# Performance work log

Measured on AMD Instinct MI355X. Metric: run time of the kernel, lower is better.

The kernel has to match this reference:

```python
import jax, jax.numpy as jnp
import numpy as np

B, L, G, N, K, E = 64, 512, 128, 32, 8, 65536
NTOK, D_TOK, H_DIR, NTL_INP, NHID, NREL = 10000, 64, 64, 32, 16, 16


def _bn(x, gamma, beta, eps=1e-5):
    # training-mode BatchNorm1d over axis 0; x: (n, C)
    mu = x.mean(0)
    var = x.var(0)
    return gamma * (x - mu) / jnp.sqrt(var + eps) + beta


def _lstm(x, w_ih, w_hh, b_ih, b_hh):
    # x: (B, T, D); torch gate order i, f, g, o
    nb = x.shape[0]
    H = w_hh.shape[1]
    def step(carry, xt):
        h, c = carry
        g = xt @ w_ih.T + b_ih + h @ w_hh.T + b_hh
        i, f, gg, o = jnp.split(g, 4, axis=-1)
        c = jax.nn.sigmoid(f) * c + jax.nn.sigmoid(i) * jnp.tanh(gg)
        h = jax.nn.sigmoid(o) * jnp.tanh(c)
        return (h, c), h
    init = (jnp.zeros((nb, H), x.dtype), jnp.zeros((nb, H), x.dtype))
    _, hs = jax.lax.scan(step, init, jnp.swapaxes(x, 0, 1))
    return jnp.swapaxes(hs, 0, 1)


def setup_inputs() -> dict:
    key = jax.random.key(0)
    ks = jax.random.split(key, 24)
    inp = {}
    inp['seq'] = jax.random.randint(ks[0], (B, L), 0, NTOK)
    inp['pos2grp'] = jax.random.randint(ks[1], (B, L), 0, G)
    inp['idx'] = jax.random.randint(ks[2], (B, N, K), 0, L)
    inp['u'] = jax.random.randint(ks[3], (E,), 0, B * N)
    inp['v'] = jax.random.randint(ks[4], (E,), 0, B * N)
    # parameters
    s = 1.0 / np.sqrt(H_DIR)
    inp['tok_emb'] = jax.random.normal(ks[5], (NTOK, D_TOK), jnp.float32)
    for tag, k0 in (('f', 6), ('b', 10)):
        inp[f'w_ih_{tag}'] = s * jax.random.normal(ks[k0], (4 * H_DIR, D_TOK), jnp.float32)
        inp[f'w_hh_{tag}'] = s * jax.random.normal(ks[k0 + 1], (4 * H_DIR, H_DIR), jnp.float32)
        inp[f'b_ih_{tag}'] = s * jax.random.normal(ks[k0 + 2], (4 * H_DIR,), jnp.float32)
        inp[f'b_hh_{tag}'] = s * jax.random.normal(ks[k0 + 3], (4 * H_DIR,), jnp.float32)
    inp['w_src'] = (1.0 / np.sqrt(2 * H_DIR)) * jax.random.normal(ks[14], (NTL_INP, 2 * H_DIR), jnp.float32)
    inp['b_src'] = jnp.zeros((NTL_INP,), jnp.float32)
    inp['w_dst'] = (1.0 / np.sqrt(2 * H_DIR)) * jax.random.normal(ks[15], (NTL_INP, 2 * H_DIR), jnp.float32)
    inp['b_dst'] = jnp.zeros((NTL_INP,), jnp.float32)
    inp['g_src'] = jnp.ones((NTL_INP,), jnp.float32)
    inp['be_src'] = jnp.zeros((NTL_INP,), jnp.float32)
    inp['g_dst'] = jnp.ones((NTL_INP,), jnp.float32)
    inp['be_dst'] = jnp.zeros((NTL_INP,), jnp.float32)
    inp['ntl_w'] = 0.001 * jax.random.normal(ks[16], (NREL, NHID, NTL_INP, NTL_INP), jnp.float32)
    inp['ntl_v'] = 0.001 * jax.random.normal(ks[17], (NREL, NHID, 2 * NTL_INP), jnp.float32)
    inp['ntl_b'] = jnp.zeros((NREL, NHID, 1), jnp.float32)
    inp['ntl_u'] = 0.001 * jax.random.normal(ks[18], (NREL, 1, NHID), jnp.float32)
    inp['ntl_g'] = jnp.ones((NREL * NHID,), jnp.float32)
    inp['ntl_be'] = jnp.zeros((NREL * NHID,), jnp.float32)
    return inp


def reference(seq, pos2grp, idx, u, v, tok_emb,
              w_ih_f, w_hh_f, b_ih_f, b_hh_f,
              w_ih_b, w_hh_b, b_ih_b, b_hh_b,
              w_src, b_src, w_dst, b_dst,
              g_src, be_src, g_dst, be_dst,
              ntl_w, ntl_v, ntl_b, ntl_u, ntl_g, ntl_be):
    # token embed + scatter-sum tokens -> groups
    x_tok = tok_emb[seq]                                   # (B, L, D)
    gid = (pos2grp + jnp.arange(B)[:, None] * G).reshape(-1)
    x_grp = jax.ops.segment_sum(x_tok.reshape(B * L, -1), gid,
                                num_segments=B * G).reshape(B, G, -1)
    # bidirectional LSTM over groups
    hf = _lstm(x_grp, w_ih_f, w_hh_f, b_ih_f, b_hh_f)
    hb = jnp.flip(_lstm(jnp.flip(x_grp, 1), w_ih_b, w_hh_b, b_ih_b, b_hh_b), 1)
    h_grp = jnp.concatenate([hf, hb], -1)                  # (B, G, 2H)
    # hierarchical gather + sum: node <- sum over K token positions' groups
    b_idx = jnp.arange(B)[:, None, None]
    g_idx = pos2grp[b_idx, idx]                            # (B, N, K)
    h = h_grp[b_idx, g_idx].sum(2).reshape(B * N, -1)      # (B*N, 2H)
    # edge endpoint projections + batchnorm
    hs = _bn(h[u] @ w_src.T + b_src, g_src, be_src)        # (E, ninp)
    ht = _bn(h[v] @ w_dst.T + b_dst, g_dst, be_dst)
    # Neural Tensor Layer
    linear = jnp.einsum('rhd,nd->rhn', ntl_v, jnp.concatenate([hs, ht], 1))
    bil = jnp.stack([
        jnp.einsum('nhj,nj->hn', jnp.einsum('ni,hij->nhj', hs, ntl_w[r]), ht)
        for r in range(NREL)], 0)                          # (R, H, E)
    z = bil + linear + ntl_b
    mu = z.mean(-1, keepdims=True)
    var = z.var(-1, keepdims=True)
    zn = ntl_g.reshape(NREL, NHID, 1) * (z - mu) / jnp.sqrt(var + 1e-5) \
         + ntl_be.reshape(NREL, NHID, 1)
    t = jnp.tanh(zn)
    logit = jnp.einsum('rh,rhn->nr', ntl_u[:, 0, :], t)    # (E, R)
    return logit
```

## Files before the change

kernel.cpp:

```cpp
#include <hip/hip_runtime.h>
#include <hip/hip_bf16.h>
#include <cstdint>

constexpr int B_   = 64;
constexpr int L_   = 512;
constexpr int G_   = 128;
constexpr int N_   = 32;
constexpr int K_   = 8;
constexpr int E_   = 65536;
constexpr int DTOK = 64;
constexpr int H_   = 64;
constexpr int NI   = 32;
constexpr int RH   = 256;
constexpr int M_   = 2048;
constexpr int JA   = 33;
constexpr int COLS = RH * JA;
constexpr int STRD = 36;

#define DEV static __device__ __forceinline__

DEV float sigm(float x) { return 1.f / (1.f + __expf(-x)); }
DEV float tanh_fast(float x) {
    x = fminf(15.f, fmaxf(-15.f, x));
    float e = __expf(2.f * x);
    return (e - 1.f) / (e + 1.f);
}

__global__ __launch_bounds__(256) void k_embed(const int* __restrict__ seq,
                                               const int* __restrict__ p2g,
                                               const float* __restrict__ emb,
                                               float* __restrict__ xg) {
    int gid = blockIdx.x * 256 + threadIdx.x;
    if (gid >= B_ * L_ * DTOK) return;
    int d  = gid & 63;
    int bl = gid >> 6;
    int b  = bl >> 9;
    int s  = seq[bl];
    int g  = p2g[bl];
    atomicAdd(&xg[((b << 7) + g) * 64 + d], emb[s * 64 + d]);
}

__global__ __launch_bounds__(256) void k_hist(const int* __restrict__ u,
                                              const int* __restrict__ v,
                                              int* __restrict__ cu, int* __restrict__ cv) {
    int n = blockIdx.x * 256 + threadIdx.x;
    if (n >= E_) return;
    atomicAdd(&cu[u[n]], 1);
    atomicAdd(&cv[v[n]], 1);
}

__global__ __launch_bounds__(256) void k_pre(const float* __restrict__ xg,
                                             const float* __restrict__ wihf,
                                             const float* __restrict__ bihf,
                                             const float* __restrict__ bhhf,
                                             const float* __restrict__ wihb,
                                             const float* __restrict__ bihb,
                                             const float* __restrict__ bhhb,
                                             float* __restrict__ pre) {
    int dir = blockIdx.y;
    int t   = threadIdx.x;
    const float* wih = dir ? wihb : wihf;
    float bias = dir ? (bihb[t] + bhhb[t]) : (bihf[t] + bhhf[t]);
    int r0 = blockIdx.x * 32;

    float4 wv[16];
#pragma unroll
    for (int c = 0; c < 16; c++) wv[c] = ((const float4*)(wih + t * 64))[c];

    __shared__ __align__(16) float xs[32][68];
    for (int tix = t; tix < 32 * 16; tix += 256) {
        int r = tix >> 4, c = tix & 15;
        ((float4*)&xs[r][0])[c] = ((const float4*)(xg + (size_t)(r0 + r) * 64))[c];
    }
    __syncthreads();

    for (int ml = 0; ml < 32; ml++) {
        float acc = bias;
        const float4* xp = (const float4*)&xs[ml][0];
#pragma unroll
        for (int c = 0; c < 16; c++) {
            float4 x4 = xp[c];
            acc += x4.x * wv[c].x + x4.y * wv[c].y + x4.z * wv[c].z + x4.w * wv[c].w;
        }
        pre[((size_t)dir * 8192 + r0 + ml) * 256 + t] = acc;
    }
}

__global__ __launch_bounds__(256) void k_lstm(const float* __restrict__ pre,
                                              const float* __restrict__ whh_f,
                                              const float* __restrict__ whh_b,
                                              float* __restrict__ hgrp) {
    int blk = blockIdx.x;
    int dir = blk >> 6;
    int b   = blk & 63;
    const float* whh = dir ? whh_b : whh_f;
    int t = threadIdx.x;

    float4 wv[16];
#pragma unroll
    for (int c = 0; c < 16; c++) wv[c] = ((const float4*)(whh + t * 64))[c];

    __shared__ __align__(16) float hl[64];
    __shared__ float cl[64];
    __shared__ float gl[256];
    if (t < 64) { hl[t] = 0.f; cl[t] = 0.f; }
    __syncthreads();

    const float* prow = pre + ((size_t)dir * 8192 + b * G_) * 256 + t;
    int s0 = dir ? (G_ - 1) : 0;
    float pnext = prow[(size_t)s0 * 256];

    for (int k = 0; k < G_; k++) {
        int s = dir ? (G_ - 1 - k) : k;
        float pcur = pnext;
        if (k + 1 < G_) {
            int sn = dir ? (G_ - 2 - k) : (k + 1);
            pnext = prow[(size_t)sn * 256];
        }
        float acc = pcur;
        const float4* hp = (const float4*)hl;
#pragma unroll
        for (int c = 0; c < 16; c++) {
            float4 h4 = hp[c];
            acc += h4.x * wv[c].x + h4.y * wv[c].y + h4.z * wv[c].z + h4.w * wv[c].w;
        }
        gl[t] = acc;
        __syncthreads();
        if (t < 64) {
            float gi = gl[t], gf = gl[64 + t], gg = gl[128 + t], go = gl[192 + t];
            float c2 = sigm(gf) * cl[t] + sigm(gi) * tanh_fast(gg);
            float hh = sigm(go) * tanh_fast(c2);
            cl[t] = c2; hl[t] = hh;
            hgrp[((size_t)b * G_ + s) * 128 + dir * 64 + t] = hh;
        }
        __syncthreads();
    }
}

__global__ __launch_bounds__(128) void k_gather(const int* __restrict__ idx,
                                                const int* __restrict__ p2g,
                                                const float* __restrict__ hgrp,
                                                float* __restrict__ hnode) {
    int m = blockIdx.x;
    int d = threadIdx.x;
    int b = m >> 5;
    float acc = 0.f;
#pragma unroll
    for (int k = 0; k < K_; k++) {
        int l = idx[m * K_ + k];
        int g = p2g[b * L_ + l];
        acc += hgrp[((size_t)b * G_ + g) * 128 + d];
    }
    hnode[(size_t)m * 128 + d] = acc;
}

__global__ __launch_bounds__(256) void k_proj(const float* __restrict__ hnode,
                                              const float* __restrict__ wsrc,
                                              const float* __restrict__ bsrc,
                                              const float* __restrict__ wdst,
                                              const float* __restrict__ bdst,
                                              float* __restrict__ Ps, float* __restrict__ Pd) {
    __shared__ __align__(16) float hsl[8][132];
    __shared__ __align__(16) float wsl[32][132];
    __shared__ __align__(16) float wdl[32][132];
    int m0 = blockIdx.x * 8;
    int t  = threadIdx.x;
    for (int tix = t; tix < 8 * 32; tix += 256) {
        int r = tix >> 5, c = tix & 31;
        ((float4*)&hsl[r][0])[c] = ((const float4*)(hnode + (size_t)(m0 + r) * 128))[c];
    }
    for (int tix = t; tix < 32 * 32; tix += 256) {
        int r = tix >> 5, c = tix & 31;
        ((float4*)&wsl[r][0])[c] = ((const float4*)(wsrc + (size_t)r * 128))[c];
        ((float4*)&wdl[r][0])[c] = ((const float4*)(wdst + (size_t)r * 128))[c];
    }
    __syncthreads();
    int ml = t >> 5, o = t & 31;
    float accS = bsrc[o], accD = bdst[o];
    const float4* hp = (const float4*)&hsl[ml][0];
    const float4* sp = (const float4*)&wsl[o][0];
    const float4* dp = (const float4*)&wdl[o][0];
#pragma unroll
    for (int c = 0; c < 32; c++) {
        float4 h4 = hp[c], s4 = sp[c], d4 = dp[c];
        accS += h4.x * s4.x + h4.y * s4.y + h4.z * s4.z + h4.w * s4.w;
        accD += h4.x * d4.x + h4.y * d4.y + h4.z * d4.z + h4.w * d4.w;
    }
    Ps[(size_t)(m0 + ml) * 32 + o] = accS;
    Pd[(size_t)(m0 + ml) * 32 + o] = accD;
}

__global__ __launch_bounds__(1024) void k_bnstat(const float* __restrict__ Ps,
                                                 const float* __restrict__ Pd,
                                                 const int* __restrict__ cu,
                                                 const int* __restrict__ cv,
                                                 float* __restrict__ bnout) {
    int side = blockIdx.x;
    const float* P  = side ? Pd : Ps;
    const int*   cn = side ? cv : cu;
    int t  = threadIdx.x;
    int mp = t >> 5, o = t & 31;
    float s1 = 0.f, s2 = 0.f;
    for (int m = mp; m < M_; m += 32) {
        float c = (float)cn[m];
        float x = P[(size_t)m * 32 + o];
        s1 += c * x;
        s2 += c * x * x;
    }
    __shared__ float r1[1024], r2[1024];
    r1[t] = s1; r2[t] = s2;
    __syncthreads();
    for (int off = 512; off >= 32; off >>= 1) {
        if (t < off) { r1[t] += r1[t + off]; r2[t] += r2[t + off]; }
        __syncthreads();
    }
    if (t < 32) {
        float mu  = r1[t] / (float)E_;
        float var = r2[t] / (float)E_ - mu * mu;
        bnout[side * 64 + t]      = mu;
        bnout[side * 64 + 32 + t] = rsqrtf(var + 1e-5f);
    }
}

__global__ __launch_bounds__(256) void k_norm(const float* __restrict__ Ps,
                                              const float* __restrict__ Pd,
                                              const float* __restrict__ bnout,
                                              const float* __restrict__ gs,
                                              const float* __restrict__ bes,
                                              const float* __restrict__ gd,
                                              const float* __restrict__ bed,
                                              float* __restrict__ hsaug,
                                              float* __restrict__ htaug) {
    int gid = blockIdx.x * 256 + threadIdx.x;
    if (gid >= M_ * 2 * STRD) return;
    int m = gid / (2 * STRD), s2 = gid % (2 * STRD);
    if (s2 < STRD) {
        int i = s2;
        float val = (i < 32) ? (gs[i] * (Ps[(size_t)m * 32 + i] - bnout[i]) * bnout[32 + i] + bes[i])
                             : ((i == 32) ? 1.f : 0.f);
        hsaug[(size_t)m * STRD + i] = val;
    } else {
        int j = s2 - STRD;
        float val = (j < 32) ? (gd[j] * (Pd[(size_t)m * 32 + j] - bnout[64 + j]) * bnout[96 + j] + bed[j])
                             : ((j == 32) ? 1.f : 0.f);
        htaug[(size_t)m * STRD + j] = val;
    }
}

__global__ __launch_bounds__(256) void k_waug(const float* __restrict__ ntlw,
                                              const float* __restrict__ ntlv,
                                              const float* __restrict__ ntlb,
                                              float* __restrict__ waug) {
    int gid = blockIdx.x * 256 + threadIdx.x;
    if (gid >= JA * COLS) return;
    int i   = gid / COLS;
    int col = gid - i * COLS;
    int rh  = col / JA;
    int j   = col - rh * JA;
    float val;
    if (i < 32) val = (j < 32) ? ntlw[((size_t)rh * 32 + i) * 32 + j] : ntlv[rh * 64 + i];
    else        val = (j == 32) ? ntlb[rh] : 0.f;
    waug[gid] = val;
}

__global__ __launch_bounds__(256) void k_agemm(const float* __restrict__ hsaug,
                                               const float* __restrict__ waug,
                                               __hip_bfloat16* __restrict__ A) {
    int mt  = blockIdx.x;
    int ct  = blockIdx.y;
    int col = ct * 256 + threadIdx.x;
    float w[JA];
#pragma unroll
    for (int i = 0; i < JA; i++) w[i] = waug[(size_t)i * COLS + col];

    __shared__ __align__(16) float hs[32][STRD];
    for (int tix = threadIdx.x; tix < 32 * 9; tix += 256) {
        int r = tix / 9, c = tix - r * 9;
        ((float4*)&hs[r][0])[c] = ((const float4*)(hsaug + (size_t)(mt * 32 + r) * STRD))[c];
    }
    __syncthreads();
#pragma unroll 1
    for (int ml = 0; ml < 32; ml++) {
        float acc = 0.f;
#pragma unroll
        for (int i = 0; i < JA; i++) acc += hs[ml][i] * w[i];
        A[(size_t)(mt * 32 + ml) * COLS + col] = __float2bfloat16(acc);
    }
}

__global__ __launch_bounds__(256) void k_ldst(const float* __restrict__ htaug,
                                              const float* __restrict__ ntlv,
                                              float* __restrict__ Ldst) {
    int m0 = blockIdx.x * 8;
    int rh = threadIdx.x;
    __shared__ __align__(16) float ht[8][STRD];
    for (int tix = threadIdx.x; tix < 8 * 9; tix += 256) {
        int r = tix / 9, c = tix - r * 9;
        ((float4*)&ht[r][0])[c] = ((const float4*)(htaug + (size_t)(m0 + r) * STRD))[c];
    }
    float w[32];
#pragma unroll
    for (int j = 0; j < 32; j++) w[j] = ntlv[rh * 64 + 32 + j];
    __syncthreads();
    for (int ml = 0; ml < 8; ml++) {
        float acc = 0.f;
#pragma unroll
        for (int j = 0; j < 32; j++) acc += ht[ml][j] * w[j];
        Ldst[(size_t)(m0 + ml) * 256 + rh] = acc;
    }
}

__global__ __launch_bounds__(1024) void k_scan(const int* __restrict__ cu,
                                               int* __restrict__ ustart,
                                               int* __restrict__ ucursor) {
    __shared__ int s[2048];
    int t  = threadIdx.x;
    int c0 = cu[t], c1 = cu[t + 1024];
    s[t] = c0; s[t + 1024] = c1;
    __syncthreads();
    for (int off = 1; off < 2048; off <<= 1) {
        int a0 = (t >= off) ? s[t - off] : 0;
        int a1 = ((t + 1024) >= off) ? s[t + 1024 - off] : 0;
        __syncthreads();
        s[t] += a0; s[t + 1024] += a1;
        __syncthreads();
    }
    int e0 = s[t] - c0, e1 = s[t + 1024] - c1;
    ustart[t] = e0;            ustart[t + 1024] = e1;
    ucursor[t] = e0;           ucursor[t + 1024] = e1;
    if (t == 0) ustart[2048] = E_;
}

__global__ __launch_bounds__(256) void k_scatter(const int* __restrict__ u,
                                                 int* __restrict__ ucursor,
                                                 int* __restrict__ eorder) {
    int n = blockIdx.x * 256 + threadIdx.x;
    if (n >= E_) return;
    int pos = atomicAdd(&ucursor[u[n]], 1);
    eorder[pos] = n;
}

__global__ __launch_bounds__(256, 2) void k_z(const __hip_bfloat16* __restrict__ A,
                                              const float* __restrict__ htaug,
                                              const float* __restrict__ Ldst,
                                              const int* __restrict__ ustart,
                                              const int* __restrict__ eorder,
                                              const int* __restrict__ v,
                                              __hip_bfloat16* __restrict__ z,
                                              float* __restrict__ zsum,
                                              float* __restrict__ zsq) {
    __shared__ __align__(16) float al[256 * STRD];
    __shared__ __align__(16) float htl[32][STRD];
    __shared__ int nnl[32], vvl[32];
    int t = threadIdx.x;
    al[t * STRD + 33] = 0.f; al[t * STRD + 34] = 0.f; al[t * STRD + 35] = 0.f;
    float s1 = 0.f, s2 = 0.f;

    for (int ui = 0; ui < 4; ui++) {
        int uu = blockIdx.x * 4 + ui;
        __syncthreads();
        for (int k = 0; k < JA; k++) {
            int idx2 = k * 256 + t;
            int rh = idx2 / JA, j = idx2 - rh * JA;
            al[rh * STRD + j] = __bfloat162float(A[(size_t)uu * COLS + idx2]);
        }
        __syncthreads();
        float4 av4[9];
#pragma unroll
        for (int c = 0; c < 9; c++) av4[c] = ((const float4*)&al[t * STRD])[c];

        int e0 = ustart[uu], e1 = ustart[uu + 1];
        for (int eb = e0; eb < e1; eb += 32) {
            int nb = min(32, e1 - eb);
            __syncthreads();
            if (t < nb) { int n = eorder[eb + t]; nnl[t] = n; vvl[t] = v[n]; }
            __syncthreads();
            for (int tix = t; tix < nb * 9; tix += 256) {
                int e = tix / 9, c = tix - e * 9;
                ((float4*)&htl[e][0])[c] = ((const float4*)(htaug + (size_t)vvl[e] * STRD))[c];
            }
            __syncthreads();
            for (int e = 0; e < nb; e++) {
                float acc = Ldst[(size_t)vvl[e] * 256 + t];
                const float4* hp = (const float4*)&htl[e][0];
#pragma unroll
                for (int c = 0; c < 9; c++) {
                    float4 h4 = hp[c];
                    acc += av4[c].x * h4.x + av4[c].y * h4.y + av4[c].z * h4.z + av4[c].w * h4.w;
                }
                z[(size_t)nnl[e] * 256 + t] = __float2bfloat16(acc);
                s1 += acc; s2 += acc * acc;
            }
        }
    }
    atomicAdd(&zsum[t], s1);
    atomicAdd(&zsq[t], s2);
}

__global__ __launch_bounds__(256) void k_lnfin(const float* __restrict__ zsum,
                                               const float* __restrict__ zsq,
                                               float* __restrict__ zstat) {
    int t = threadIdx.x;
    float mu  = zsum[t] / (float)E_;
    float var = zsq[t] / (float)E_ - mu * mu;
    zstat[t]       = mu;
    zstat[256 + t] = rsqrtf(var + 1e-5f);
}

__global__ __launch_bounds__(256) void k_logit(const __hip_bfloat16* __restrict__ z,
                                               const float* __restrict__ zstat,
                                               const float* __restrict__ ntlu,
                                               const float* __restrict__ ntlg,
                                               const float* __restrict__ ntlbe,
                                               float* __restrict__ out) {
    int t  = threadIdx.x;
    int n0 = blockIdx.x * 16;
    float mu  = zstat[t], isd = zstat[256 + t];
    float g   = ntlg[t],  be  = ntlbe[t];
    float uw  = ntlu[t];
    float zv[16];
#pragma unroll
    for (int nl = 0; nl < 16; nl++)
        zv[nl] = __bfloat162float(z[(size_t)(n0 + nl) * 256 + t]);
#pragma unroll 1
    for (int nl = 0; nl < 16; nl++) {
        float zn  = g * (zv[nl] - mu) * isd + be;
        float val = uw * tanhf(zn);
        val += __shfl_xor(val, 1);
        val += __shfl_xor(val, 2);
        val += __shfl_xor(val, 4);
        val += __shfl_xor(val, 8);
        if ((t & 15) == 0) out[(size_t)(n0 + nl) * 16 + (t >> 4)] = val;
    }
}

extern "C" void kernel_launch(void* const* d_in, const int* in_sizes, int n_in,
                              void* d_out, int out_size, void* d_ws, size_t ws_size,
                              hipStream_t stream) {
    const int*   seq   = (const int*)d_in[0];
    const int*   p2g   = (const int*)d_in[1];
    const int*   idx   = (const int*)d_in[2];
    const int*   u     = (const int*)d_in[3];
    const int*   v     = (const int*)d_in[4];
    const float* emb   = (const float*)d_in[5];
    const float* wihf  = (const float*)d_in[6];
    const float* whhf  = (const float*)d_in[7];
    const float* bihf  = (const float*)d_in[8];
    const float* bhhf  = (const float*)d_in[9];
    const float* wihb  = (const float*)d_in[10];
    const float* whhb  = (const float*)d_in[11];
    const float* bihb  = (const float*)d_in[12];
    const float* bhhb  = (const float*)d_in[13];
    const float* wsrc  = (const float*)d_in[14];
    const float* bsrc  = (const float*)d_in[15];
    const float* wdst  = (const float*)d_in[16];
    const float* bdst  = (const float*)d_in[17];
    const float* gs    = (const float*)d_in[18];
    const float* bes   = (const float*)d_in[19];
    const float* gd    = (const float*)d_in[20];
    const float* bed   = (const float*)d_in[21];
    const float* ntlw  = (const float*)d_in[22];
    const float* ntlv  = (const float*)d_in[23];
    const float* ntlb  = (const float*)d_in[24];
    const float* ntlu  = (const float*)d_in[25];
    const float* ntlg  = (const float*)d_in[26];
    const float* ntlbe = (const float*)d_in[27];
    float* out = (float*)d_out;

    char* ws = (char*)d_ws;
    size_t off = 0;
    auto take = [&](size_t bytes) -> char* {
        char* p = ws + off;
        off = (off + bytes + 255) & ~(size_t)255;
        return p;
    };
    float* x_grp  = (float*)take((size_t)B_ * G_ * 64 * 4);
    int*   cnt_u  = (int*)  take(2048 * 4);
    int*   cnt_v  = (int*)  take(2048 * 4);
    float* zsum   = (float*)take(256 * 4);
    float* zsq    = (float*)take(256 * 4);
    size_t zero_bytes = off;
    int*   ucursor = (int*)  take(2048 * 4);
    int*   ustart  = (int*)  take(2049 * 4);
    int*   eorder  = (int*)  take((size_t)E_ * 4);
    float* pre     = (float*)take((size_t)2 * 8192 * 256 * 4);
    float* hgrp    = (float*)take((size_t)B_ * G_ * 128 * 4);
    float* hnode   = (float*)take((size_t)M_ * 128 * 4);
    float* Psrc    = (float*)take((size_t)M_ * 32 * 4);
    float* Pdst    = (float*)take((size_t)M_ * 32 * 4);
    float* bnout   = (float*)take(128 * 4);
    float* hsaug   = (float*)take((size_t)M_ * STRD * 4);
    float* htaug   = (float*)take((size_t)M_ * STRD * 4);
    float* waug    = (float*)take((size_t)JA * COLS * 4);
    float* LdstB   = (float*)take((size_t)M_ * 256 * 4);
    float* zstat   = (float*)take(512 * 4);
    __hip_bfloat16* Abuf = (__hip_bfloat16*)take((size_t)M_ * COLS * 2);
    __hip_bfloat16* zbuf = (__hip_bfloat16*)take((size_t)E_ * 256 * 2);
    (void)ws_size; (void)in_sizes; (void)n_in; (void)out_size;

    hipMemsetAsync(d_ws, 0, zero_bytes, stream);

    k_embed<<<(B_ * L_ * DTOK) / 256, 256, 0, stream>>>(seq, p2g, emb, x_grp);
    k_hist<<<E_ / 256, 256, 0, stream>>>(u, v, cnt_u, cnt_v);
    k_pre<<<dim3(256, 2), 256, 0, stream>>>(x_grp, wihf, bihf, bhhf, wihb, bihb, bhhb, pre);
    k_lstm<<<128, 256, 0, stream>>>(pre, whhf, whhb, hgrp);
    k_gather<<<M_, 128, 0, stream>>>(idx, p2g, hgrp, hnode);
    k_proj<<<M_ / 8, 256, 0, stream>>>(hnode, wsrc, bsrc, wdst, bdst, Psrc, Pdst);
    k_bnstat<<<2, 1024, 0, stream>>>(Psrc, Pdst, cnt_u, cnt_v, bnout);
    k_norm<<<(M_ * 2 * STRD + 255) / 256, 256, 0, stream>>>(Psrc, Pdst, bnout, gs, bes, gd, bed, hsaug, htaug);
    k_waug<<<(JA * COLS + 255) / 256, 256, 0, stream>>>(ntlw, ntlv, ntlb, waug);
    k_agemm<<<dim3(M_ / 32, JA), 256, 0, stream>>>(hsaug, waug, Abuf);
    k_ldst<<<M_ / 8, 256, 0, stream>>>(htaug, ntlv, LdstB);
    k_scan<<<1, 1024, 0, stream>>>(cnt_u, ustart, ucursor);
    k_scatter<<<E_ / 256, 256, 0, stream>>>(u, ucursor, eorder);
    k_z<<<M_ / 4, 256, 0, stream>>>(Abuf, htaug, LdstB, ustart, eorder, v, zbuf, zsum, zsq);
    k_lnfin<<<1, 256, 0, stream>>>(zsum, zsq, zstat);
    k_logit<<<E_ / 16, 256, 0, stream>>>(zbuf, zstat, ntlu, ntlg, ntlbe, out);
}
```

Baseline: 422.1 us.

## Fuse small kernels, restructure LSTM step with lane permutes, fold ldst into waug

Merges embed+hist, pre+scan, lstm+scatter, norm+waug and lnfin+logit into combined launches, cutting the number of kernel launches. The embedding sum now accumulates per batch in shared memory rather than through global atomics. The LSTM step gathers the four gates through ds_bpermute, keeps the cell state in registers and double-buffers h, so each step needs one barrier instead of two. The destination-linear term is folded into the augmented weight row (the constant-1 column), which removes the Ldst kernel and its buffer. The logit kernel uses the fast tanh approximation, which adds a small accuracy risk.

```diff
diff --git a/kernel.cpp b/kernel.cpp
--- a/kernel.cpp
+++ b/kernel.cpp
@@ -10,7 +10,6 @@
 constexpr int E_   = 65536;
 constexpr int DTOK = 64;
 constexpr int H_   = 64;
-constexpr int NI   = 32;
 constexpr int RH   = 256;
 constexpr int M_   = 2048;
 constexpr int JA   = 33;
@@ -25,28 +24,37 @@
     float e = __expf(2.f * x);
     return (e - 1.f) / (e + 1.f);
 }
-
-__global__ __launch_bounds__(256) void k_embed(const int* __restrict__ seq,
-                                               const int* __restrict__ p2g,
-                                               const float* __restrict__ emb,
-                                               float* __restrict__ xg) {
-    int gid = blockIdx.x * 256 + threadIdx.x;
-    if (gid >= B_ * L_ * DTOK) return;
-    int d  = gid & 63;
-    int bl = gid >> 6;
-    int b  = bl >> 9;
-    int s  = seq[bl];
-    int g  = p2g[bl];
-    atomicAdd(&xg[((b << 7) + g) * 64 + d], emb[s * 64 + d]);
-}
-
-__global__ __launch_bounds__(256) void k_hist(const int* __restrict__ u,
-                                              const int* __restrict__ v,
-                                              int* __restrict__ cu, int* __restrict__ cv) {
-    int n = blockIdx.x * 256 + threadIdx.x;
-    if (n >= E_) return;
-    atomicAdd(&cu[u[n]], 1);
-    atomicAdd(&cv[v[n]], 1);
+DEV float bperm(float x, int srclane) {
+    return __int_as_float(__builtin_amdgcn_ds_bpermute(srclane << 2, __float_as_int(x)));
+}
+
+__global__ __launch_bounds__(256) void k_eh(const int* __restrict__ seq,
+                                            const int* __restrict__ p2g,
+                                            const float* __restrict__ emb,
+                                            const int* __restrict__ u,
+                                            const int* __restrict__ v,
+                                            float* __restrict__ xg,
+                                            int* __restrict__ cu, int* __restrict__ cv) {
+    int blk = blockIdx.x;
+    int t   = threadIdx.x;
+    if (blk >= 64) {
+        int n = (blk - 64) * 256 + t;
+        atomicAdd(&cu[u[n]], 1);
+        atomicAdd(&cv[v[n]], 1);
+        return;
+    }
+    __shared__ float xgl[G_ * 64];
+    for (int i = t; i < G_ * 64; i += 256) xgl[i] = 0.f;
+    __syncthreads();
+    int b = blk;
+    int d = t & 63, part = t >> 6;
+    for (int l = part; l < L_; l += 4) {
+        int s = seq[b * L_ + l];
+        int g = p2g[b * L_ + l];
+        atomicAdd(&xgl[g * 64 + d], emb[s * 64 + d]);
+    }
+    __syncthreads();
+    for (int i = t; i < G_ * 64; i += 256) xg[(size_t)b * G_ * 64 + i] = xgl[i];
 }
 
 __global__ __launch_bounds__(256) void k_pre(const float* __restrict__ xg,
@@ -56,18 +64,44 @@
                                              const float* __restrict__ wihb,
                                              const float* __restrict__ bihb,
                                              const float* __restrict__ bhhb,
-                                             float* __restrict__ pre) {
-    int dir = blockIdx.y;
+                                             float* __restrict__ pre,
+                                             const int* __restrict__ cu,
+                                             int* __restrict__ ustart,
+                                             int* __restrict__ ucursor) {
+    int blk = blockIdx.x;
     int t   = threadIdx.x;
+    __shared__ __align__(16) float xs[32][68];
+    __shared__ int ps[256];
+    if (blk == 512) {
+        int base = t * 8, run = 0;
+        int c[8], loc[8];
+#pragma unroll
+        for (int i = 0; i < 8; i++) c[i] = cu[base + i];
+#pragma unroll
+        for (int i = 0; i < 8; i++) { loc[i] = run; run += c[i]; }
+        ps[t] = run;
+        __syncthreads();
+        for (int off = 1; off < 256; off <<= 1) {
+            int a = (t >= off) ? ps[t - off] : 0;
+            __syncthreads();
+            ps[t] += a;
+            __syncthreads();
+        }
+        int ex = ps[t] - run;
+#pragma unroll
+        for (int i = 0; i < 8; i++) { ustart[base + i] = ex + loc[i]; ucursor[base + i] = ex + loc[i]; }
+        if (t == 255) ustart[2048] = E_;
+        return;
+    }
+    int dir = blk >> 8;
     const float* wih = dir ? wihb : wihf;
     float bias = dir ? (bihb[t] + bhhb[t]) : (bihf[t] + bhhf[t]);
-    int r0 = blockIdx.x * 32;
+    int r0 = (blk & 255) * 32;
 
     float4 wv[16];
 #pragma unroll
     for (int c = 0; c < 16; c++) wv[c] = ((const float4*)(wih + t * 64))[c];
 
-    __shared__ __align__(16) float xs[32][68];
     for (int tix = t; tix < 32 * 16; tix += 256) {
         int r = tix >> 4, c = tix & 15;
         ((float4*)&xs[r][0])[c] = ((const float4*)(xg + (size_t)(r0 + r) * 64))[c];
@@ -86,29 +120,43 @@
     }
 }
 
-__global__ __launch_bounds__(256) void k_lstm(const float* __restrict__ pre,
-                                              const float* __restrict__ whh_f,
-                                              const float* __restrict__ whh_b,
-                                              float* __restrict__ hgrp) {
+__global__ __launch_bounds__(256) void k_ls(const float* __restrict__ pre,
+                                            const float* __restrict__ whh_f,
+                                            const float* __restrict__ whh_b,
+                                            float* __restrict__ hgrp,
+                                            const int* __restrict__ u,
+                                            int* __restrict__ ucursor,
+                                            int* __restrict__ eorder) {
     int blk = blockIdx.x;
+    int t   = threadIdx.x;
+    if (blk >= 128) {
+        int n = (blk - 128) * 256 + t;
+        int pos = atomicAdd(&ucursor[u[n]], 1);
+        eorder[pos] = n;
+        return;
+    }
     int dir = blk >> 6;
     int b   = blk & 63;
     const float* whh = dir ? whh_b : whh_f;
-    int t = threadIdx.x;
+    int l = t & 63;
+    int w = t >> 6;
+    int q = l >> 4;
+    int e = (w << 4) + (l & 15);
+    int grow = (q << 6) + e;
 
     float4 wv[16];
 #pragma unroll
-    for (int c = 0; c < 16; c++) wv[c] = ((const float4*)(whh + t * 64))[c];
-
-    __shared__ __align__(16) float hl[64];
-    __shared__ float cl[64];
-    __shared__ float gl[256];
-    if (t < 64) { hl[t] = 0.f; cl[t] = 0.f; }
-    __syncthreads();
-
-    const float* prow = pre + ((size_t)dir * 8192 + b * G_) * 256 + t;
+    for (int c = 0; c < 16; c++) wv[c] = ((const float4*)(whh + grow * 64))[c];
+
+    __shared__ __align__(16) float hl[2][64];
+    if (t < 64) hl[0][t] = 0.f;
+    float creg = 0.f;
+    __syncthreads();
+
+    const float* prow = pre + ((size_t)dir * 8192 + b * G_) * 256 + grow;
     int s0 = dir ? (G_ - 1) : 0;
     float pnext = prow[(size_t)s0 * 256];
+    int bi = l & 15;
 
     for (int k = 0; k < G_; k++) {
         int s = dir ? (G_ - 1 - k) : k;
@@ -117,21 +165,27 @@
             int sn = dir ? (G_ - 2 - k) : (k + 1);
             pnext = prow[(size_t)sn * 256];
         }
-        float acc = pcur;
-        const float4* hp = (const float4*)hl;
-#pragma unroll
-        for (int c = 0; c < 16; c++) {
-            float4 h4 = hp[c];
-            acc += h4.x * wv[c].x + h4.y * wv[c].y + h4.z * wv[c].z + h4.w * wv[c].w;
-        }
-        gl[t] = acc;
-        __syncthreads();
-        if (t < 64) {
-            float gi = gl[t], gf = gl[64 + t], gg = gl[128 + t], go = gl[192 + t];
-            float c2 = sigm(gf) * cl[t] + sigm(gi) * tanh_fast(gg);
-            float hh = sigm(go) * tanh_fast(c2);
-            cl[t] = c2; hl[t] = hh;
-            hgrp[((size_t)b * G_ + s) * 128 + dir * 64 + t] = hh;
+        const float4* hp = (const float4*)hl[k & 1];
+        float a0 = 0.f, a1 = 0.f, a2 = 0.f, a3 = 0.f;
+#pragma unroll
+        for (int c = 0; c < 16; c += 4) {
+            float4 h0 = hp[c], h1 = hp[c + 1], h2 = hp[c + 2], h3 = hp[c + 3];
+            a0 += h0.x * wv[c].x     + h0.y * wv[c].y     + h0.z * wv[c].z     + h0.w * wv[c].w;
+            a1 += h1.x * wv[c + 1].x + h1.y * wv[c + 1].y + h1.z * wv[c + 1].z + h1.w * wv[c + 1].w;
+            a2 += h2.x * wv[c + 2].x + h2.y * wv[c + 2].y + h2.z * wv[c + 2].z + h2.w * wv[c + 2].w;
+            a3 += h3.x * wv[c + 3].x + h3.y * wv[c + 3].y + h3.z * wv[c + 3].z + h3.w * wv[c + 3].w;
+        }
+        float g = pcur + ((a0 + a1) + (a2 + a3));
+        float gi = bperm(g, bi);
+        float gf = bperm(g, bi + 16);
+        float gG = bperm(g, bi + 32);
+        float go = bperm(g, bi + 48);
+        float c2 = sigm(gf) * creg + sigm(gi) * tanh_fast(gG);
+        float hh = sigm(go) * tanh_fast(c2);
+        creg = c2;
+        if (q == 0) {
+            hl[(k + 1) & 1][e] = hh;
+            hgrp[((size_t)b * G_ + s) * 128 + dir * 64 + e] = hh;
         }
         __syncthreads();
     }
@@ -222,44 +276,45 @@
     }
 }
 
-__global__ __launch_bounds__(256) void k_norm(const float* __restrict__ Ps,
+__global__ __launch_bounds__(256) void k_prep(const float* __restrict__ Ps,
                                               const float* __restrict__ Pd,
                                               const float* __restrict__ bnout,
                                               const float* __restrict__ gs,
                                               const float* __restrict__ bes,
                                               const float* __restrict__ gd,
                                               const float* __restrict__ bed,
-                                              float* __restrict__ hsaug,
-                                              float* __restrict__ htaug) {
-    int gid = blockIdx.x * 256 + threadIdx.x;
-    if (gid >= M_ * 2 * STRD) return;
-    int m = gid / (2 * STRD), s2 = gid % (2 * STRD);
-    if (s2 < STRD) {
-        int i = s2;
-        float val = (i < 32) ? (gs[i] * (Ps[(size_t)m * 32 + i] - bnout[i]) * bnout[32 + i] + bes[i])
-                             : ((i == 32) ? 1.f : 0.f);
-        hsaug[(size_t)m * STRD + i] = val;
-    } else {
-        int j = s2 - STRD;
-        float val = (j < 32) ? (gd[j] * (Pd[(size_t)m * 32 + j] - bnout[64 + j]) * bnout[96 + j] + bed[j])
-                             : ((j == 32) ? 1.f : 0.f);
-        htaug[(size_t)m * STRD + j] = val;
-    }
-}
-
-__global__ __launch_bounds__(256) void k_waug(const float* __restrict__ ntlw,
+                                              const float* __restrict__ ntlw,
                                               const float* __restrict__ ntlv,
                                               const float* __restrict__ ntlb,
+                                              float* __restrict__ hsaug,
+                                              float* __restrict__ htaug,
                                               float* __restrict__ waug) {
-    int gid = blockIdx.x * 256 + threadIdx.x;
-    if (gid >= JA * COLS) return;
+    int blk = blockIdx.x;
+    int t   = threadIdx.x;
+    if (blk < 576) {
+        int gid = blk * 256 + t;
+        int m = gid / (2 * STRD), s2 = gid % (2 * STRD);
+        if (s2 < STRD) {
+            int i = s2;
+            float val = (i < 32) ? (gs[i] * (Ps[(size_t)m * 32 + i] - bnout[i]) * bnout[32 + i] + bes[i])
+                                 : ((i == 32) ? 1.f : 0.f);
+            hsaug[(size_t)m * STRD + i] = val;
+        } else {
+            int j = s2 - STRD;
+            float val = (j < 32) ? (gd[j] * (Pd[(size_t)m * 32 + j] - bnout[64 + j]) * bnout[96 + j] + bed[j])
+                                 : ((j == 32) ? 1.f : 0.f);
+            htaug[(size_t)m * STRD + j] = val;
+        }
+        return;
+    }
+    int gid = (blk - 576) * 256 + t;
     int i   = gid / COLS;
     int col = gid - i * COLS;
     int rh  = col / JA;
     int j   = col - rh * JA;
     float val;
     if (i < 32) val = (j < 32) ? ntlw[((size_t)rh * 32 + i) * 32 + j] : ntlv[rh * 64 + i];
-    else        val = (j == 32) ? ntlb[rh] : 0.f;
+    else        val = (j < 32) ? ntlv[rh * 64 + 32 + j] : ntlb[rh];
     waug[gid] = val;
 }
 
@@ -288,61 +343,8 @@
     }
 }
 
-__global__ __launch_bounds__(256) void k_ldst(const float* __restrict__ htaug,
-                                              const float* __restrict__ ntlv,
-                                              float* __restrict__ Ldst) {
-    int m0 = blockIdx.x * 8;
-    int rh = threadIdx.x;
-    __shared__ __align__(16) float ht[8][STRD];
-    for (int tix = threadIdx.x; tix < 8 * 9; tix += 256) {
-        int r = tix / 9, c = tix - r * 9;
-        ((float4*)&ht[r][0])[c] = ((const float4*)(htaug + (size_t)(m0 + r) * STRD))[c];
-    }
-    float w[32];
-#pragma unroll
-    for (int j = 0; j < 32; j++) w[j] = ntlv[rh * 64 + 32 + j];
-    __syncthreads();
-    for (int ml = 0; ml < 8; ml++) {
-        float acc = 0.f;
-#pragma unroll
-        for (int j = 0; j < 32; j++) acc += ht[ml][j] * w[j];
-        Ldst[(size_t)(m0 + ml) * 256 + rh] = acc;
-    }
-}
-
-__global__ __launch_bounds__(1024) void k_scan(const int* __restrict__ cu,
-                                               int* __restrict__ ustart,
-                                               int* __restrict__ ucursor) {
-    __shared__ int s[2048];
-    int t  = threadIdx.x;
-    int c0 = cu[t], c1 = cu[t + 1024];
-    s[t] = c0; s[t + 1024] = c1;
-    __syncthreads();
-    for (int off = 1; off < 2048; off <<= 1) {
-        int a0 = (t >= off) ? s[t - off] : 0;
-        int a1 = ((t + 1024) >= off) ? s[t + 1024 - off] : 0;
-        __syncthreads();
-        s[t] += a0; s[t + 1024] += a1;
-        __syncthreads();
-    }
-    int e0 = s[t] - c0, e1 = s[t + 1024] - c1;
-    ustart[t] = e0;            ustart[t + 1024] = e1;
-    ucursor[t] = e0;           ucursor[t + 1024] = e1;
-    if (t == 0) ustart[2048] = E_;
-}
-
-__global__ __launch_bounds__(256) void k_scatter(const int* __restrict__ u,
-                                                 int* __restrict__ ucursor,
-                                                 int* __restrict__ eorder) {
-    int n = blockIdx.x * 256 + threadIdx.x;
-    if (n >= E_) return;
-    int pos = atomicAdd(&ucursor[u[n]], 1);
-    eorder[pos] = n;
-}
-
 __global__ __launch_bounds__(256, 2) void k_z(const __hip_bfloat16* __restrict__ A,
                                               const float* __restrict__ htaug,
-                                              const float* __restrict__ Ldst,
                                               const int* __restrict__ ustart,
                                               const int* __restrict__ eorder,
                                               const int* __restrict__ v,
@@ -381,7 +383,7 @@
             }
             __syncthreads();
             for (int e = 0; e < nb; e++) {
-                float acc = Ldst[(size_t)vvl[e] * 256 + t];
+                float acc = 0.f;
                 const float4* hp = (const float4*)&htl[e][0];
 #pragma unroll
                 for (int c = 0; c < 9; c++) {
@@ -397,25 +399,18 @@
     atomicAdd(&zsq[t], s2);
 }
 
-__global__ __launch_bounds__(256) void k_lnfin(const float* __restrict__ zsum,
+__global__ __launch_bounds__(256) void k_logit(const __hip_bfloat16* __restrict__ z,
+                                               const float* __restrict__ zsum,
                                                const float* __restrict__ zsq,
-                                               float* __restrict__ zstat) {
-    int t = threadIdx.x;
-    float mu  = zsum[t] / (float)E_;
-    float var = zsq[t] / (float)E_ - mu * mu;
-    zstat[t]       = mu;
-    zstat[256 + t] = rsqrtf(var + 1e-5f);
-}
-
-__global__ __launch_bounds__(256) void k_logit(const __hip_bfloat16* __restrict__ z,
-                                               const float* __restrict__ zstat,
                                                const float* __restrict__ ntlu,
                                                const float* __restrict__ ntlg,
                                                const float* __restrict__ ntlbe,
                                                float* __restrict__ out) {
     int t  = threadIdx.x;
     int n0 = blockIdx.x * 16;
-    float mu  = zstat[t], isd = zstat[256 + t];
+    float mu  = zsum[t] / (float)E_;
+    float var = zsq[t] / (float)E_ - mu * mu;
+    float isd = rsqrtf(var + 1e-5f);
     float g   = ntlg[t],  be  = ntlbe[t];
     float uw  = ntlu[t];
     float zv[16];
@@ -425,7 +420,7 @@
 #pragma unroll 1
     for (int nl = 0; nl < 16; nl++) {
         float zn  = g * (zv[nl] - mu) * isd + be;
-        float val = uw * tanhf(zn);
+        float val = uw * tanh_fast(zn);
         val += __shfl_xor(val, 1);
         val += __shfl_xor(val, 2);
         val += __shfl_xor(val, 4);
@@ -474,12 +469,12 @@
         off = (off + bytes + 255) & ~(size_t)255;
         return p;
     };
-    float* x_grp  = (float*)take((size_t)B_ * G_ * 64 * 4);
     int*   cnt_u  = (int*)  take(2048 * 4);
     int*   cnt_v  = (int*)  take(2048 * 4);
     float* zsum   = (float*)take(256 * 4);
     float* zsq    = (float*)take(256 * 4);
     size_t zero_bytes = off;
+    float* x_grp   = (float*)take((size_t)B_ * G_ * 64 * 4);
     int*   ucursor = (int*)  take(2048 * 4);
     int*   ustart  = (int*)  take(2049 * 4);
     int*   eorder  = (int*)  take((size_t)E_ * 4);
@@ -492,28 +487,22 @@
     float* hsaug   = (float*)take((size_t)M_ * STRD * 4);
     float* htaug   = (float*)take((size_t)M_ * STRD * 4);
     float* waug    = (float*)take((size_t)JA * COLS * 4);
-    float* LdstB   = (float*)take((size_t)M_ * 256 * 4);
-    float* zstat   = (float*)take(512 * 4);
     __hip_bfloat16* Abuf = (__hip_bfloat16*)take((size_t)M_ * COLS * 2);
     __hip_bfloat16* zbuf = (__hip_bfloat16*)take((size_t)E_ * 256 * 2);
     (void)ws_size; (void)in_sizes; (void)n_in; (void)out_size;
 
     hipMemsetAsync(d_ws, 0, zero_bytes, stream);
 
-    k_embed<<<(B_ * L_ * DTOK) / 256, 256, 0, stream>>>(seq, p2g, emb, x_grp);
-    k_hist<<<E_ / 256, 256, 0, stream>>>(u, v, cnt_u, cnt_v);
-    k_pre<<<dim3(256, 2), 256, 0, stream>>>(x_grp, wihf, bihf, bhhf, wihb, bihb, bhhb, pre);
-    k_lstm<<<128, 256, 0, stream>>>(pre, whhf, whhb, hgrp);
+    k_eh<<<320, 256, 0, stream>>>(seq, p2g, emb, u, v, x_grp, cnt_u, cnt_v);
+    k_pre<<<513, 256, 0, stream>>>(x_grp, wihf, bihf, bhhf, wihb, bihb, bhhb, pre,
+                                   cnt_u, ustart, ucursor);
+    k_ls<<<384, 256, 0, stream>>>(pre, whhf, whhb, hgrp, u, ucursor, eorder);
     k_gather<<<M_, 128, 0, stream>>>(idx, p2g, hgrp, hnode);
     k_proj<<<M_ / 8, 256, 0, stream>>>(hnode, wsrc, bsrc, wdst, bdst, Psrc, Pdst);
     k_bnstat<<<2, 1024, 0, stream>>>(Psrc, Pdst, cnt_u, cnt_v, bnout);
-    k_norm<<<(M_ * 2 * STRD + 255) / 256, 256, 0, stream>>>(Psrc, Pdst, bnout, gs, bes, gd, bed, hsaug, htaug);
-    k_waug<<<(JA * COLS + 255) / 256, 256, 0, stream>>>(ntlw, ntlv, ntlb, waug);
+    k_prep<<<576 + 1089, 256, 0, stream>>>(Psrc, Pdst, bnout, gs, bes, gd, bed,
+                                           ntlw, ntlv, ntlb, hsaug, htaug, waug);
     k_agemm<<<dim3(M_ / 32, JA), 256, 0, stream>>>(hsaug, waug, Abuf);
-    k_ldst<<<M_ / 8, 256, 0, stream>>>(htaug, ntlv, LdstB);
-    k_scan<<<1, 1024, 0, stream>>>(cnt_u, ustart, ucursor);
-    k_scatter<<<E_ / 256, 256, 0, stream>>>(u, ucursor, eorder);
-    k_z<<<M_ / 4, 256, 0, stream>>>(Abuf, htaug, LdstB, ustart, eorder, v, zbuf, zsum, zsq);
-    k_lnfin<<<1, 256, 0, stream>>>(zsum, zsq, zstat);
-    k_logit<<<E_ / 16, 256, 0, stream>>>(zbuf, zstat, ntlu, ntlg, ntlbe, out);
-}
+    k_z<<<M_ / 4, 256, 0, stream>>>(Abuf, htaug, ustart, eorder, v, zbuf, zsum, zsq);
+    k_logit<<<E_ / 16, 256, 0, stream>>>(zbuf, zsum, zsq, ntlu, ntlg, ntlbe, out);
+}
```

Result: slower. 443.5 us (+5.1%).
